# Kernel optimization log

Hardware: AMD Instinct MI355X
Metric: run time of the kernel (lower is better)

## Reference

```python
import jax, jax.numpy as jnp
import numpy as np

B, S, D_MODEL, D_HEAD = 4, 4096, 768, 64

def setup_inputs() -> dict:
    key = jax.random.key(0)
    kx, kq, kk, kv = jax.random.split(key, 4)
    scale = 1.0 / np.sqrt(D_MODEL)
    return {
        "x": jax.random.normal(kx, (B, S, D_MODEL), dtype=jnp.float32),
        "W_Q": jax.random.normal(kq, (D_MODEL, D_HEAD), dtype=jnp.float32) * scale,
        "W_K": jax.random.normal(kk, (D_MODEL, D_HEAD), dtype=jnp.float32) * scale,
        "W_V": jax.random.normal(kv, (D_MODEL, D_HEAD), dtype=jnp.float32) * scale,
    }

def reference(x, W_Q, W_K, W_V):
    # x: [B, S, d_model]; projections to [B, S, d_head]
    Q = x @ W_Q
    K = x @ W_K
    V = x @ W_V
    d_head = Q.shape[-1]
    # scores: [B, S, S], scaled dot product
    A = jnp.einsum('bid,bjd->bij', Q, K) / jnp.sqrt(jnp.asarray(d_head, Q.dtype))
    S_len = x.shape[1]
    causal = jnp.tril(jnp.ones((S_len, S_len), dtype=bool))
    A = jnp.where(causal[None, :, :], A, -jnp.inf)
    A = jax.nn.softmax(A, axis=-1)
    return jnp.einsum('bij,bjd->bid', A, V)
```

## Files before the change

kernel.cpp:

```cpp
#include <hip/hip_runtime.h>
#include <hip/hip_bf16.h>

typedef __bf16 bf16_t;
typedef bf16_t bf16x8 __attribute__((ext_vector_type(8)));
typedef float f32x4 __attribute__((ext_vector_type(4)));
typedef float f32x16 __attribute__((ext_vector_type(16)));
typedef unsigned int u32;

#define NB 4
#define SS 4096
#define DM 768
#define DH 64
#define NROW (NB * SS)
#define CSCALE (0.125f * 1.44269504088896341f)
#define MFIX 24.0f

#define QOFF 0u
#define KOFF 2097152u
#define VOFF 4194304u
#define WOFF 6291456u

#define SB() __builtin_amdgcn_sched_barrier(0)

__device__ __forceinline__ u32 cvtpk_bf16(float lo, float hi) {
    u32 r;
    asm volatile("v_cvt_pk_bf16_f32 %0, %1, %2" : "=v"(r) : "v"(lo), "v"(hi));
    return r;
}

__global__ __launch_bounds__(256) void wt_kernel(const float* __restrict__ wq,
                                                 const float* __restrict__ wk,
                                                 const float* __restrict__ wv,
                                                 bf16_t* __restrict__ wt) {
    int id = blockIdx.x * 256 + threadIdx.x;
    if (id >= 3 * DM * DH) return;
    int m = id / (DM * DH);
    int r = id - m * (DM * DH);
    int k = r >> 6;
    int c = r & 63;
    const float* w = (m == 0) ? wq : (m == 1) ? wk : wv;
    wt[(size_t)m * DH * DM + (size_t)c * DM + k] = (bf16_t)w[k * DH + c];
}

__global__ __launch_bounds__(512, 4) void proj_kernel(const float* __restrict__ x,
                                                      const bf16_t* __restrict__ wt,
                                                      bf16_t* __restrict__ Qo,
                                                      bf16_t* __restrict__ Ko,
                                                      bf16_t* __restrict__ Vt) {
    __shared__ __align__(16) float xs[4][2048];

    const int tid = threadIdx.x;
    const int lane = tid & 63;
    const int wid = tid >> 6;
    const int wr = wid & 1;
    const int wc = wid >> 1;
    const int l15 = lane & 15;
    const int g = lane >> 4;
    const int m0 = blockIdx.x * 32;

    const int srow = tid >> 4;
    const int skc = (tid & 15) ^ (srow & 7);
    const float* sbase = x + (size_t)(m0 + srow) * DM + skc * 4;

    #define STAGE(bsel, t_)                                                         \
        __builtin_amdgcn_global_load_lds(                                           \
            (const __attribute__((address_space(1))) void*)(sbase + (t_) * 64),     \
            (__attribute__((address_space(3))) void*)(&xs[bsel][wid * 256]),        \
            16, 0, 0);

    size_t wbase[3];
    #pragma unroll
    for (int n = 0; n < 3; n++) {
        const int gn = wc * 3 + n;
        const int mm = gn >> 2;
        const int cj = gn & 3;
        wbase[n] = (size_t)mm * DH * DM + (size_t)(cj * 16 + l15) * DM + g * 8;
    }

    f32x4 acc[3];
    #pragma unroll
    for (int n = 0; n < 3; n++)
        #pragma unroll
        for (int j = 0; j < 4; j++) acc[n][j] = 0.0f;

    const int arow = wr * 16 + l15;
    int roff[2][2];
    #pragma unroll
    for (int kk = 0; kk < 2; kk++)
        #pragma unroll
        for (int c = 0; c < 2; c++)
            roff[kk][c] = arow * 64 + ((kk * 8 + g * 2 + c) ^ (arow & 7)) * 4;

    bf16x8 wslot[3][3][2];

    #pragma unroll
    for (int n = 0; n < 3; n++)
        #pragma unroll
        for (int kk = 0; kk < 2; kk++)
            wslot[0][n][kk] = *reinterpret_cast<const bf16x8*>(wt + wbase[n] + kk * 32);
    SB();
    STAGE(0, 0); SB();
    #pragma unroll
    for (int n = 0; n < 3; n++)
        #pragma unroll
        for (int kk = 0; kk < 2; kk++)
            wslot[1][n][kk] = *reinterpret_cast<const bf16x8*>(wt + wbase[n] + 64 + kk * 32);
    SB();
    STAGE(1, 1); SB();
    STAGE(2, 2); SB();
    asm volatile("s_waitcnt vmcnt(8)");
    SB();
    __builtin_amdgcn_s_barrier();
    SB();

    #pragma unroll
    for (int t = 0; t < 12; t++) {
        if (t + 2 < 12) {
            #pragma unroll
            for (int n = 0; n < 3; n++)
                #pragma unroll
                for (int kk = 0; kk < 2; kk++)
                    wslot[(t + 2) % 3][n][kk] = *reinterpret_cast<const bf16x8*>(
                        wt + wbase[n] + (t + 2) * 64 + kk * 32);
        }
        SB();
        if (t + 3 < 12) { STAGE((t + 3) & 3, t + 3); }
        SB();
        bf16x8 a[2];
        #pragma unroll
        for (int kk = 0; kk < 2; kk++) {
            f32x4 c0 = *reinterpret_cast<const f32x4*>(&xs[t & 3][roff[kk][0]]);
            f32x4 c1 = *reinterpret_cast<const f32x4*>(&xs[t & 3][roff[kk][1]]);
            bf16x8 tt;
            #pragma unroll
            for (int j = 0; j < 4; j++) { tt[j] = (bf16_t)c0[j]; tt[4 + j] = (bf16_t)c1[j]; }
            a[kk] = tt;
        }
        #pragma unroll
        for (int n = 0; n < 3; n++)
            #pragma unroll
            for (int kk = 0; kk < 2; kk++)
                acc[n] = __builtin_amdgcn_mfma_f32_16x16x32_bf16(a[kk], wslot[t % 3][n][kk], acc[n], 0, 0, 0);

        if (t < 11) {
            if (t <= 8)       { asm volatile("s_waitcnt vmcnt(8)"); }
            else if (t == 9)  { asm volatile("s_waitcnt vmcnt(7)"); }
            else              { asm volatile("s_waitcnt vmcnt(0)"); }
            SB();
            __builtin_amdgcn_s_barrier();
            SB();
        }
    }
    #undef STAGE

    #pragma unroll
    for (int n = 0; n < 3; n++) {
        const int gn = wc * 3 + n;
        const int mm = gn >> 2;
        const int cj = gn & 3;
        #pragma unroll
        for (int j = 0; j < 4; j++) {
            int row = m0 + wr * 16 + g * 4 + j;
            int col = cj * 16 + l15;
            float v = acc[n][j];
            if (mm == 0)      Qo[(size_t)row * DH + col] = (bf16_t)(v * CSCALE);
            else if (mm == 1) Ko[(size_t)row * DH + col] = (bf16_t)v;
            else              Vt[(size_t)col * NROW + row] = (bf16_t)v;
        }
    }
}

__global__ __launch_bounds__(256, 2) void attn_kernel(const bf16_t* __restrict__ Q,
                                                      const bf16_t* __restrict__ K,
                                                      const bf16_t* __restrict__ Vt,
                                                      float* __restrict__ out) {
    __shared__ float Ob[2][2][16][64];
    __shared__ float Ls[2][64];

    const int tid = threadIdx.x;
    const int lane = tid & 63;
    const int w = tid >> 6;
    const int l31 = lane & 31;
    const int hi = lane >> 5;
    const int bx = blockIdx.x;
    const int b = (bx & 7) >> 1;
    const int r_ = (bx >> 3) * 2 + (bx & 1);
    const int tile = (r_ < 64) ? (127 - r_) : (r_ - 64);
    const int q0 = tile * 32;
    const int nkv = (tile >> 1) + 1;
    const int q = q0 + l31;

    const bf16_t* Qb = Q + (size_t)b * SS * DH;
    const bf16_t* Kb = K + (size_t)b * SS * DH;
    const bf16_t* Vb = Vt + (size_t)b * SS;

    bf16x8 bq[4];
    #pragma unroll
    for (int ks = 0; ks < 4; ks++)
        bq[ks] = *reinterpret_cast<const bf16x8*>(
            Qb + (size_t)(q0 + l31) * DH + ks * 16 + hi * 8);

    f32x16 o[2];
    #pragma unroll
    for (int c = 0; c < 2; c++)
        #pragma unroll
        for (int r = 0; r < 16; r++) o[c][r] = 0.0f;
    float lsum = 0.0f;

    for (int kt = w; kt < nkv; kt += 4) {
        const int kv0 = kt * 64;
        const bool diag = (kv0 + 63 > q0);

        bf16x8 ak0[4];
        #pragma unroll
        for (int ks = 0; ks < 4; ks++)
            ak0[ks] = *reinterpret_cast<const bf16x8*>(
                Kb + (size_t)(kv0 + l31) * DH + ks * 16 + hi * 8);
        SB();
        bf16x8 ak1[4];
        #pragma unroll
        for (int ks = 0; ks < 4; ks++)
            ak1[ks] = *reinterpret_cast<const bf16x8*>(
                Kb + (size_t)(kv0 + 32 + l31) * DH + ks * 16 + hi * 8);
        SB();
        bf16x8 vf[2][4];
        #pragma unroll
        for (int c = 0; c < 2; c++)
            #pragma unroll
            for (int kks = 0; kks < 4; kks++)
                vf[c][kks] = *reinterpret_cast<const bf16x8*>(
                    Vb + (size_t)(c * 32 + l31) * NROW + kv0 + kks * 16 + hi * 8);
        SB();

        u32 pa[4][4];
        f32x16 s0;
        #pragma unroll
        for (int r = 0; r < 16; r++) s0[r] = 0.0f;
        #pragma unroll
        for (int ks = 0; ks < 4; ks++)
            s0 = __builtin_amdgcn_mfma_f32_32x32x16_bf16(ak0[ks], bq[ks], s0, 0, 0, 0);
        f32x16 s1;
        #pragma unroll
        for (int r = 0; r < 16; r++) s1[r] = 0.0f;
        #pragma unroll
        for (int ks = 0; ks < 4; ks++)
            s1 = __builtin_amdgcn_mfma_f32_32x32x16_bf16(ak1[ks], bq[ks], s1, 0, 0, 0);

        #pragma unroll
        for (int blk = 0; blk < 2; blk++) {
            const f32x16& s = blk ? s1 : s0;
            const int kvbase = kv0 + blk * 32 + 4 * hi;
            float p[16];
            #pragma unroll
            for (int r = 0; r < 16; r++) {
                float e = exp2f(s[r] - MFIX);
                if (diag) {
                    int kv = kvbase + (r & 3) + 8 * (r >> 2);
                    e = (kv > q) ? 0.0f : e;
                }
                p[r] = e;
                lsum += e;
            }
            #pragma unroll
            for (int ks2 = 0; ks2 < 2; ks2++) {
                u32 w01 = cvtpk_bf16(p[8 * ks2 + 0], p[8 * ks2 + 1]);
                u32 w23 = cvtpk_bf16(p[8 * ks2 + 2], p[8 * ks2 + 3]);
                u32 w45 = cvtpk_bf16(p[8 * ks2 + 4], p[8 * ks2 + 5]);
                u32 w67 = cvtpk_bf16(p[8 * ks2 + 6], p[8 * ks2 + 7]);
                asm volatile("v_permlane32_swap_b32 %0, %1" : "+v"(w01), "+v"(w45));
                asm volatile("v_permlane32_swap_b32 %0, %1" : "+v"(w23), "+v"(w67));
                pa[blk * 2 + ks2][0] = w01;
                pa[blk * 2 + ks2][1] = w23;
                pa[blk * 2 + ks2][2] = w45;
                pa[blk * 2 + ks2][3] = w67;
            }
        }

        #pragma unroll
        for (int kks = 0; kks < 4; kks++) {
            union { u32 w4[4]; bf16x8 v; } uu;
            uu.w4[0] = pa[kks][0];
            uu.w4[1] = pa[kks][1];
            uu.w4[2] = pa[kks][2];
            uu.w4[3] = pa[kks][3];
            #pragma unroll
            for (int c = 0; c < 2; c++)
                o[c] = __builtin_amdgcn_mfma_f32_32x32x16_bf16(uu.v, vf[c][kks], o[c], 0, 0, 0);
        }
    }

    if (w >= 2) {
        #pragma unroll
        for (int c = 0; c < 2; c++)
            #pragma unroll
            for (int r = 0; r < 16; r++) Ob[w - 2][c][r][lane] = o[c][r];
        Ls[w - 2][lane] = lsum;
    }
    __syncthreads();
    if (w < 2) {
        #pragma unroll
        for (int c = 0; c < 2; c++)
            #pragma unroll
            for (int r = 0; r < 16; r++) o[c][r] += Ob[w][c][r][lane];
        lsum += Ls[w][lane];
    }
    __syncthreads();
    if (w == 1) {
        #pragma unroll
        for (int c = 0; c < 2; c++)
            #pragma unroll
            for (int r = 0; r < 16; r++) Ob[0][c][r][lane] = o[c][r];
        Ls[0][lane] = lsum;
    }
    __syncthreads();
    if (w == 0) {
        #pragma unroll
        for (int c = 0; c < 2; c++)
            #pragma unroll
            for (int r = 0; r < 16; r++) o[c][r] += Ob[0][c][r][lane];
        lsum += Ls[0][lane];

        float lfull = lsum + __shfl_xor(lsum, 32);
        float* ob = out + ((size_t)b * SS + q0) * DH;
        #pragma unroll
        for (int c = 0; c < 2; c++)
            #pragma unroll
            for (int r = 0; r < 16; r++) {
                const int qr = (r & 3) + 8 * (r >> 2) + 4 * hi;
                float lr = __shfl(lfull, qr);
                ob[(size_t)qr * DH + c * 32 + l31] = o[c][r] / lr;
            }
    }
}

extern "C" void kernel_launch(void* const* d_in, const int* in_sizes, int n_in,
                              void* d_out, int out_size, void* d_ws, size_t ws_size,
                              hipStream_t stream) {
    const float* x  = (const float*)d_in[0];
    const float* wq = (const float*)d_in[1];
    const float* wk = (const float*)d_in[2];
    const float* wv = (const float*)d_in[3];
    float* out = (float*)d_out;

    char* ws = (char*)d_ws;
    bf16_t* Qw = (bf16_t*)(ws + QOFF);
    bf16_t* Kw = (bf16_t*)(ws + KOFF);
    bf16_t* Vt = (bf16_t*)(ws + VOFF);
    bf16_t* Wt = (bf16_t*)(ws + WOFF);

    hipLaunchKernelGGL(wt_kernel, dim3((3 * DM * DH + 255) / 256), dim3(256), 0, stream,
                       wq, wk, wv, Wt);
    hipLaunchKernelGGL(proj_kernel, dim3(NROW / 32), dim3(512), 0, stream,
                       x, Wt, Qw, Kw, Vt);
    hipLaunchKernelGGL(attn_kernel, dim3(NB * 128), dim3(256), 0, stream,
                       Qw, Kw, Vt, out);
}
```

Baseline: 81.68 us.

## Halve projection block to 4 waves, each wave covering both 16-row tiles

The projection kernel now runs 256 threads per block instead of 512. Each wave computes both 16-row halves of the 32-row tile, so each loaded W fragment feeds two MFMAs and the block issues half as many weight loads. Each thread stages two x chunks per step, and the vmcnt waits are adjusted to match. The softmax scale is folded into W_Q during the transpose kernel, removing a per-element multiply in the epilogue. In exchange, each wave holds more accumulators and A fragments, which raises register pressure and leaves fewer waves per block to hide latency.

New measurement: 66.96 us (median of 16 runs). -18.0%, faster.

```diff
diff --git a/kernel.cpp b/kernel.cpp
--- a/kernel.cpp
+++ b/kernel.cpp
@@ -39,10 +39,12 @@
     int k = r >> 6;
     int c = r & 63;
     const float* w = (m == 0) ? wq : (m == 1) ? wk : wv;
-    wt[(size_t)m * DH * DM + (size_t)c * DM + k] = (bf16_t)w[k * DH + c];
-}
-
-__global__ __launch_bounds__(512, 4) void proj_kernel(const float* __restrict__ x,
+    float v = w[k * DH + c];
+    if (m == 0) v *= CSCALE;
+    wt[(size_t)m * DH * DM + (size_t)c * DM + k] = (bf16_t)v;
+}
+
+__global__ __launch_bounds__(256, 3) void proj_kernel(const float* __restrict__ x,
                                                       const bf16_t* __restrict__ wt,
                                                       bf16_t* __restrict__ Qo,
                                                       bf16_t* __restrict__ Ko,
@@ -52,44 +54,50 @@
     const int tid = threadIdx.x;
     const int lane = tid & 63;
     const int wid = tid >> 6;
-    const int wr = wid & 1;
-    const int wc = wid >> 1;
     const int l15 = lane & 15;
     const int g = lane >> 4;
     const int m0 = blockIdx.x * 32;
 
-    const int srow = tid >> 4;
-    const int skc = (tid & 15) ^ (srow & 7);
-    const float* sbase = x + (size_t)(m0 + srow) * DM + skc * 4;
-
-    #define STAGE(bsel, t_)                                                         \
+    const int srow0 = tid >> 4;
+    const int skc0 = (tid & 15) ^ (srow0 & 7);
+    const int srow1 = 16 + srow0;
+    const int skc1 = (tid & 15) ^ (srow1 & 7);
+    const float* sb0 = x + (size_t)(m0 + srow0) * DM + skc0 * 4;
+    const float* sb1 = x + (size_t)(m0 + srow1) * DM + skc1 * 4;
+
+    #define STAGE(bsel, t_) do {                                                    \
         __builtin_amdgcn_global_load_lds(                                           \
-            (const __attribute__((address_space(1))) void*)(sbase + (t_) * 64),     \
+            (const __attribute__((address_space(1))) void*)(sb0 + (t_) * 64),       \
             (__attribute__((address_space(3))) void*)(&xs[bsel][wid * 256]),        \
-            16, 0, 0);
+            16, 0, 0);                                                              \
+        __builtin_amdgcn_global_load_lds(                                           \
+            (const __attribute__((address_space(1))) void*)(sb1 + (t_) * 64),       \
+            (__attribute__((address_space(3))) void*)(&xs[bsel][1024 + wid * 256]), \
+            16, 0, 0); } while (0)
 
     size_t wbase[3];
     #pragma unroll
     for (int n = 0; n < 3; n++) {
-        const int gn = wc * 3 + n;
+        const int gn = wid * 3 + n;
         const int mm = gn >> 2;
         const int cj = gn & 3;
         wbase[n] = (size_t)mm * DH * DM + (size_t)(cj * 16 + l15) * DM + g * 8;
     }
 
-    f32x4 acc[3];
-    #pragma unroll
-    for (int n = 0; n < 3; n++)
-        #pragma unroll
-        for (int j = 0; j < 4; j++) acc[n][j] = 0.0f;
-
-    const int arow = wr * 16 + l15;
+    f32x4 acc[2][3];
+    #pragma unroll
+    for (int fi = 0; fi < 2; fi++)
+        #pragma unroll
+        for (int n = 0; n < 3; n++)
+            #pragma unroll
+            for (int j = 0; j < 4; j++) acc[fi][n][j] = 0.0f;
+
     int roff[2][2];
     #pragma unroll
     for (int kk = 0; kk < 2; kk++)
         #pragma unroll
         for (int c = 0; c < 2; c++)
-            roff[kk][c] = arow * 64 + ((kk * 8 + g * 2 + c) ^ (arow & 7)) * 4;
+            roff[kk][c] = l15 * 64 + ((kk * 8 + g * 2 + c) ^ (l15 & 7)) * 4;
 
     bf16x8 wslot[3][3][2];
 
@@ -108,7 +116,7 @@
     SB();
     STAGE(1, 1); SB();
     STAGE(2, 2); SB();
-    asm volatile("s_waitcnt vmcnt(8)");
+    asm volatile("s_waitcnt vmcnt(10)");
     SB();
     __builtin_amdgcn_s_barrier();
     SB();
@@ -126,26 +134,31 @@
         SB();
         if (t + 3 < 12) { STAGE((t + 3) & 3, t + 3); }
         SB();
-        bf16x8 a[2];
-        #pragma unroll
-        for (int kk = 0; kk < 2; kk++) {
-            f32x4 c0 = *reinterpret_cast<const f32x4*>(&xs[t & 3][roff[kk][0]]);
-            f32x4 c1 = *reinterpret_cast<const f32x4*>(&xs[t & 3][roff[kk][1]]);
-            bf16x8 tt;
-            #pragma unroll
-            for (int j = 0; j < 4; j++) { tt[j] = (bf16_t)c0[j]; tt[4 + j] = (bf16_t)c1[j]; }
-            a[kk] = tt;
-        }
+        bf16x8 a[2][2];
+        #pragma unroll
+        for (int fi = 0; fi < 2; fi++)
+            #pragma unroll
+            for (int kk = 0; kk < 2; kk++) {
+                f32x4 c0 = *reinterpret_cast<const f32x4*>(&xs[t & 3][fi * 1024 + roff[kk][0]]);
+                f32x4 c1 = *reinterpret_cast<const f32x4*>(&xs[t & 3][fi * 1024 + roff[kk][1]]);
+                bf16x8 tt;
+                #pragma unroll
+                for (int j = 0; j < 4; j++) { tt[j] = (bf16_t)c0[j]; tt[4 + j] = (bf16_t)c1[j]; }
+                a[fi][kk] = tt;
+            }
         #pragma unroll
         for (int n = 0; n < 3; n++)
             #pragma unroll
             for (int kk = 0; kk < 2; kk++)
-                acc[n] = __builtin_amdgcn_mfma_f32_16x16x32_bf16(a[kk], wslot[t % 3][n][kk], acc[n], 0, 0, 0);
+                #pragma unroll
+                for (int fi = 0; fi < 2; fi++)
+                    acc[fi][n] = __builtin_amdgcn_mfma_f32_16x16x32_bf16(
+                        a[fi][kk], wslot[t % 3][n][kk], acc[fi][n], 0, 0, 0);
 
         if (t < 11) {
-            if (t <= 8)       { asm volatile("s_waitcnt vmcnt(8)"); }
-            else if (t == 9)  { asm volatile("s_waitcnt vmcnt(7)"); }
-            else              { asm volatile("s_waitcnt vmcnt(0)"); }
+            if (t <= 8)       { asm volatile("s_waitcnt vmcnt(10)"); }
+            else if (t == 9)  { asm volatile("s_waitcnt vmcnt(8)");  }
+            else              { asm volatile("s_waitcnt vmcnt(0)");  }
             SB();
             __builtin_amdgcn_s_barrier();
             SB();
@@ -155,18 +168,20 @@
 
     #pragma unroll
     for (int n = 0; n < 3; n++) {
-        const int gn = wc * 3 + n;
+        const int gn = wid * 3 + n;
         const int mm = gn >> 2;
         const int cj = gn & 3;
         #pragma unroll
-        for (int j = 0; j < 4; j++) {
-            int row = m0 + wr * 16 + g * 4 + j;
-            int col = cj * 16 + l15;
-            float v = acc[n][j];
-            if (mm == 0)      Qo[(size_t)row * DH + col] = (bf16_t)(v * CSCALE);
-            else if (mm == 1) Ko[(size_t)row * DH + col] = (bf16_t)v;
-            else              Vt[(size_t)col * NROW + row] = (bf16_t)v;
-        }
+        for (int fi = 0; fi < 2; fi++)
+            #pragma unroll
+            for (int j = 0; j < 4; j++) {
+                int row = m0 + fi * 16 + g * 4 + j;
+                int col = cj * 16 + l15;
+                float v = acc[fi][n][j];
+                if (mm == 0)      Qo[(size_t)row * DH + col] = (bf16_t)v;
+                else if (mm == 1) Ko[(size_t)row * DH + col] = (bf16_t)v;
+                else              Vt[(size_t)col * NROW + row] = (bf16_t)v;
+            }
     }
 }
 
@@ -350,7 +365,7 @@
 
     hipLaunchKernelGGL(wt_kernel, dim3((3 * DM * DH + 255) / 256), dim3(256), 0, stream,
                        wq, wk, wv, Wt);
-    hipLaunchKernelGGL(proj_kernel, dim3(NROW / 32), dim3(512), 0, stream,
+    hipLaunchKernelGGL(proj_kernel, dim3(NROW / 32), dim3(256), 0, stream,
                        x, Wt, Qw, Kw, Vt);
     hipLaunchKernelGGL(attn_kernel, dim3(NB * 128), dim3(256), 0, stream,
                        Qw, Kw, Vt, out);
```
